# Performance work log

Hardware: AMD Instinct MI355X
Metric: run time of the kernel (lower is better)

The kernel has to match this reference:

```python
import jax, jax.numpy as jnp
import numpy as np

B, N, C_IN, C_EMB, G = 16, 1024, 16, 64, 128
NEG = -1e12


def _lap(m):
    # m @ D^-1/2, transpose, @ D^-1/2  (matches torch code incl. transpose)
    d = jnp.sum(m, axis=1) ** -0.5
    return (m * d[None, :]).T * d[None, :]


def setup_inputs():
    key = jax.random.key(0)
    ks = jax.random.split(key, 16)
    f = jax.random.normal
    return {
        'x': f(ks[0], (B, C_IN, N), jnp.float32),
        'ct': f(ks[1], (B, C_EMB, N), jnp.float32),
        'graph_data': jax.random.uniform(ks[2], (2, N, N), dtype=jnp.float32),
        'emb_w': f(ks[3], (C_EMB, C_IN)) / np.sqrt(C_IN).astype(np.float32),
        'emb_b': f(ks[4], (C_EMB,)) * 0.01,
        'emb2_w': f(ks[5], (N, N)) / np.sqrt(N).astype(np.float32),
        'emb2_b': f(ks[6], (N,)) * 0.01,
        'att_W': f(ks[7], (C_EMB, C_EMB)) / np.sqrt(C_EMB).astype(np.float32),
        'att_a': f(ks[8], (2 * C_EMB, 1)) / np.sqrt(2 * C_EMB).astype(np.float32),
        'att_GL': f(ks[9], (N, G)) / np.sqrt(G).astype(np.float32),
        'uai_w': f(ks[10], (C_EMB, C_EMB)) / np.sqrt(C_EMB).astype(np.float32),
        'uai_b': f(ks[11], (C_EMB,)) * 0.01,
        'lin1_w': f(ks[12], (C_EMB, C_EMB)) / np.sqrt(C_EMB).astype(np.float32),
        'lin2_w': f(ks[13], (C_EMB, C_EMB)) / np.sqrt(C_EMB).astype(np.float32),
        'lin2_b': f(ks[14], (C_EMB,)) * 0.01,
        'ln_w': jnp.ones((C_EMB, N), jnp.float32),
        'ln_b': jnp.zeros((C_EMB, N), jnp.float32),
    }


def reference(x, ct, graph_data, emb_w, emb_b, emb2_w, emb2_b, att_W, att_a,
              att_GL, uai_w, uai_b, lin1_w, lin2_w, lin2_b, ln_w, ln_b):
    # emb: Conv1d k=1 -> leaky_relu -> Linear over node axis N
    h0 = jax.nn.leaky_relu(jnp.einsum('bcn,ec->ben', x, emb_w) + emb_b[None, :, None])
    h0 = jnp.einsum('ben,mn->bem', h0, emb2_w) + emb2_b[None, None, :]
    inp = jnp.swapaxes(h0, 1, 2)  # [B,N,C']

    # InterpositionAttention (repeat/cat factorized: e_ij = leakyrelu(a1.h_i + a2.h_j))
    eye = jnp.eye(N, dtype=x.dtype)
    adj_att = jax.nn.softmax(jax.nn.relu(att_GL @ att_GL.T), axis=-1) + eye
    h = inp @ att_W  # [B,N,C']
    e = jax.nn.leaky_relu((h @ att_a[:C_EMB]) + jnp.swapaxes(h @ att_a[C_EMB:], 1, 2))  # [B,N,N]
    att = jax.nn.softmax(jnp.where(adj_att > 0, e, NEG), axis=2)
    x_att = jnp.swapaxes(jax.nn.relu(att @ h), 1, 2)  # [B,C',N]

    # UAI module (eval mode: dropout off -> all MC samples equal -> sigma = 0)
    mu = jnp.swapaxes(x_att, 1, 2) @ uai_w.T + uai_b  # [B,N,C']
    x_uai = jnp.swapaxes(mu, 1, 2)  # [B,C',N]

    g1 = _lap(graph_data[0] + eye)
    g2 = _lap(graph_data[1] + eye)

    # learned adjacency from pairwise squared distances (cdist p=2, squared)
    xf = jnp.swapaxes(x_uai, 1, 2)  # [B,N,C']
    sq = jnp.sum(xf * xf, axis=-1)
    d2 = jnp.maximum(sq[:, :, None] + sq[:, None, :] - 2.0 * (xf @ jnp.swapaxes(xf, 1, 2)), 0.0)
    gl = jax.nn.softmax(jnp.exp(-d2 / (2.0 * C_EMB)) + eye, axis=-1)  # sigma^2 = emb_size

    def ln(z):  # LayerNorm over last two dims [C', N]
        m = jnp.mean(z, axis=(1, 2), keepdims=True)
        v = jnp.var(z, axis=(1, 2), keepdims=True)
        return (z - m) / jnp.sqrt(v + 1e-5) * ln_w + ln_b

    l1 = lambda z: jnp.einsum('oc,bcn->bon', lin1_w, z)
    l2 = lambda z: jnp.einsum('oc,bcn->bon', lin2_w, z) + lin2_b[None, :, None]

    x_new = ln(l1(x_uai) @ gl + l1(l1(x_uai) @ g1) @ g2)
    ft = jax.nn.gelu(ln(l2(x_uai) @ gl + l2(l2(x_uai) @ g1) @ g2), approximate=False)
    rt = ft  # rt is computed by the identical expression (dropout off)

    ct_new = ft * ct + x_new - ft * x_new
    ht = rt * jax.nn.elu(ct_new) + x_uai - rt * x_uai
    return (ht, ct_new)
```

## Files before the change

### kernel.cpp

```cpp
#include <hip/hip_runtime.h>
#include <math.h>

typedef unsigned short u16;
typedef __attribute__((ext_vector_type(8))) short short8;
typedef __attribute__((ext_vector_type(4))) float floatx4;

constexpr int BATCH = 16;
constexpr int NI = 1024;
constexpr int CE = 64;
constexpr int CI = 16;
constexpr long long NN2  = (long long)NI * NI;
constexpr long long BCN  = (long long)BATCH * CE * NI;
constexpr long long BNv  = (long long)BATCH * NI;
constexpr long long BNN  = (long long)BATCH * NI * NI;
constexpr long long S1 = (long long)CE * NI;
constexpr long long S2 = 2 * S1;

__device__ __forceinline__ float lrelu01(float x) { return x > 0.f ? x : 0.01f * x; }

__device__ __forceinline__ u16 f2bf(float f) {
  unsigned u = __builtin_bit_cast(unsigned, f);
  return (u16)((u + 0x7fffu + ((u >> 16) & 1u)) >> 16);
}
__device__ __forceinline__ float bf2f(u16 h) {
  unsigned u = ((unsigned)h) << 16;
  return __builtin_bit_cast(float, u);
}
__device__ __forceinline__ unsigned fkey(float f) {
  unsigned u = __builtin_bit_cast(unsigned, f);
  return (u & 0x80000000u) ? ~u : (u | 0x80000000u);
}
__device__ __forceinline__ float funkey(unsigned k) {
  unsigned u = (k & 0x80000000u) ? (k & 0x7fffffffu) : ~k;
  return __builtin_bit_cast(float, u);
}

template<int BM, int BN, int MODE>
__global__ __launch_bounds__(256) void mgemm(
    const u16* __restrict__ Ag, const u16* __restrict__ B1g, const u16* __restrict__ B2g,
    int K1, int K, int lda, int ldb, long long bsA, long long bsB1,
    float* __restrict__ Cf, u16* __restrict__ Cb, int ldc, long long bsC,
    const float* __restrict__ aux1, const float* __restrict__ aux2,
    const float* __restrict__ aux3, const float* __restrict__ aux4,
    float* __restrict__ Zout)
{
  constexpr int RM = BM / 2, RN = BN / 2, MI = RM / 16, NJ = RN / 16;
  __shared__ __align__(16) u16 As[BM * 64];
  __shared__ __align__(16) u16 Bs[BN * 64];
  const int z = blockIdx.z;
  const int n0 = blockIdx.x * BN;
  const int r0 = blockIdx.y * BM;
  const u16* Ab = Ag + (long long)z * bsA + (long long)r0 * lda;
  const u16* Bb1 = B1g + (long long)z * bsB1 + (long long)n0 * ldb;
  const int tid = threadIdx.x;
  const int lane = tid & 63;
  const int wid = tid >> 6;
  const int wr = wid >> 1, wc = wid & 1;
  const int q = lane >> 4, mlow = lane & 15;

  floatx4 acc[MI][NJ] = {};

  for (int k0 = 0; k0 < K; k0 += 64) {
    const u16* Asrc = Ab + k0;
    const u16* Bsrc = (k0 < K1) ? (Bb1 + k0)
                                : (B2g + (long long)n0 * ldb + (k0 - K1));
#pragma unroll
    for (int s = 0; s < (BM * 8) / 256; s++) {
      int cid = tid + s * 256;
      int r = cid >> 3, craw = cid & 7;
      uint4 v = *(const uint4*)(Asrc + (long long)r * lda + craw * 8);
      *(uint4*)&As[(r * 8 + (craw ^ (r & 7))) * 8] = v;
    }
#pragma unroll
    for (int s = 0; s < (BN * 8) / 256; s++) {
      int cid = tid + s * 256;
      int r = cid >> 3, craw = cid & 7;
      uint4 v = *(const uint4*)(Bsrc + (long long)r * ldb + craw * 8);
      *(uint4*)&Bs[(r * 8 + (craw ^ (r & 7))) * 8] = v;
    }
    __syncthreads();
#pragma unroll
    for (int kh = 0; kh < 2; kh++) {
      const int kc = kh * 4 + q;
      short8 afr[MI], bfr[NJ];
#pragma unroll
      for (int i = 0; i < MI; i++) {
        int row = wr * RM + i * 16 + mlow;
        afr[i] = *(const short8*)&As[(row * 8 + (kc ^ (row & 7))) * 8];
      }
#pragma unroll
      for (int j = 0; j < NJ; j++) {
        int row = wc * RN + j * 16 + mlow;
        bfr[j] = *(const short8*)&Bs[(row * 8 + (kc ^ (row & 7))) * 8];
      }
#pragma unroll
      for (int i = 0; i < MI; i++)
#pragma unroll
        for (int j = 0; j < NJ; j++)
          acc[i][j] = __builtin_amdgcn_mfma_f32_16x16x32_bf16(afr[i], bfr[j], acc[i][j], 0, 0, 0);
    }
    __syncthreads();
  }

  if constexpr (MODE == 3) {
    const float* sqb = aux1 + (long long)z * NI;
#pragma unroll
    for (int i = 0; i < MI; i++) {
#pragma unroll
      for (int rg = 0; rg < 4; rg++) {
        int r = r0 + wr * RM + i * 16 + q * 4 + rg;
        float sqi = sqb[r];
        float rsum = 0.f;
#pragma unroll
        for (int j = 0; j < NJ; j++) {
          int ncol = n0 + wc * RN + j * 16 + mlow;
          float d2 = fmaxf(sqi + sqb[ncol] - 2.f * acc[i][j][rg], 0.f);
          float w = __expf(__expf(-d2 * (1.f / 128.f)) + (r == ncol ? 1.f : 0.f) - 2.f);
          Cb[(long long)z * bsC + (long long)r * ldc + ncol] = f2bf(w);
          rsum += w;
        }
        rsum += __shfl_xor(rsum, 1);
        rsum += __shfl_xor(rsum, 2);
        rsum += __shfl_xor(rsum, 4);
        rsum += __shfl_xor(rsum, 8);
        if (mlow == 0) atomicAdd(&Zout[(long long)z * NI + r], rsum);
      }
    }
  } else if constexpr (MODE == 2) {
#pragma unroll
    for (int i = 0; i < MI; i++) {
#pragma unroll
      for (int rg = 0; rg < 4; rg++) {
        int r = r0 + wr * RM + i * 16 + q * 4 + rg;
        float sqp = 0.f;
#pragma unroll
        for (int j = 0; j < NJ; j++) {
          int ncol = n0 + wc * RN + j * 16 + mlow;
          float v = acc[i][j][rg] + aux1[ncol];
          long long ix = (long long)z * bsC + (long long)r * ldc + ncol;
          Cf[ix] = v;
          Cb[ix] = f2bf(v);
          sqp = fmaf(v, v, sqp);
        }
        sqp += __shfl_xor(sqp, 1);
        sqp += __shfl_xor(sqp, 2);
        sqp += __shfl_xor(sqp, 4);
        sqp += __shfl_xor(sqp, 8);
        if (mlow == 0) atomicAdd(&Zout[(long long)z * NI + r], sqp);
      }
    }
  } else {
#pragma unroll
    for (int i = 0; i < MI; i++) {
#pragma unroll
      for (int j = 0; j < NJ; j++) {
#pragma unroll
        for (int rg = 0; rg < 4; rg++) {
          int r = r0 + wr * RM + i * 16 + q * 4 + rg;
          int ncol = n0 + wc * RN + j * 16 + mlow;
          float v = acc[i][j][rg];
          if constexpr (MODE == 1) {
            v *= aux1[(long long)z * NI + r];
            v = fmaxf(v, 0.f);
            Cb[(long long)z * bsC + (long long)r * ldc + ncol] = f2bf(v);
          } else if constexpr (MODE == 4) {
            int blk = r >> 6, oo = r & 63;
            int drow = ((blk & 1) << 6) + oo;
            if (blk < 2) v = v / aux1[(long long)z * NI + ncol];
            Cb[(long long)z * bsC + (long long)drow * 2048 + (long long)(blk >> 1) * 1024 + ncol] =
                f2bf(v);
          } else if constexpr (MODE == 5) {
            v += aux3[r] * aux1[(long long)z * NI + ncol] + aux4[r] * aux2[ncol];
            Cf[(long long)z * bsC + (long long)r * ldc + ncol] = v;
          } else if constexpr (MODE == 6) {
            Cb[(long long)z * bsC + (long long)r * ldc + ncol] = f2bf(v);
          } else if constexpr (MODE == 9) {
            v += aux3[r];
            Cb[(long long)z * bsC + (long long)r * ldc + ncol] = f2bf(v);
          }
        }
      }
    }
  }
}

__global__ __launch_bounds__(256) void lap_rowsum(const float* __restrict__ gd,
                                                  float* __restrict__ dr)
{
  const int ki = blockIdx.x;
  const float* row = gd + (long long)ki * NI;
  float s = 0.f;
  for (int j = threadIdx.x; j < NI; j += 256) s += row[j];
  __shared__ float red[256];
  red[threadIdx.x] = s; __syncthreads();
  for (int st = 128; st > 0; st >>= 1) {
    if (threadIdx.x < st) red[threadIdx.x] += red[threadIdx.x + st];
    __syncthreads();
  }
  if (threadIdx.x == 0) dr[ki] = rsqrtf(red[0] + 1.f);
}

__global__ __launch_bounds__(256) void mega_prep(
    const float* __restrict__ l1w, const float* __restrict__ l2w,
    const float* __restrict__ l2b, const float* __restrict__ uaiw,
    const float* __restrict__ attW,
    u16* __restrict__ stack4, float* __restrict__ rb2ext, float* __restrict__ rl2ext,
    u16* __restrict__ uaiw_bf, u16* __restrict__ attwT_bf,
    const float* __restrict__ emb2w, u16* __restrict__ emb2w_bf,
    const float* __restrict__ x, const float* __restrict__ ew,
    const float* __restrict__ eb, u16* __restrict__ h0a,
    const float* __restrict__ gd, const float* __restrict__ dsum,
    u16* __restrict__ g2t, u16* __restrict__ g1,
    float* __restrict__ cs1)
{
  __shared__ float sm[1088];
  const int bid = blockIdx.x;
  const int t = threadIdx.x;
  if (bid < 97) {
    const int gid = bid * 256 + t;
    if (gid < 4096) {
      stack4[gid] = f2bf(l1w[gid]);
    } else if (gid < 8192) {
      stack4[gid] = f2bf(l2w[gid - 4096]);
    } else if (gid < 12288) {
      int tt = gid - 8192, o = tt >> 6, m = tt & 63;
      float s = 0.f;
      for (int c = 0; c < 64; c++) s = fmaf(l1w[o * 64 + c], l1w[c * 64 + m], s);
      stack4[gid] = f2bf(s);
    } else if (gid < 16384) {
      int tt = gid - 12288, o = tt >> 6, m = tt & 63;
      float s = 0.f;
      for (int c = 0; c < 64; c++) s = fmaf(l2w[o * 64 + c], l2w[c * 64 + m], s);
      stack4[gid] = f2bf(s);
    } else if (gid < 16512) {
      int r = gid - 16384;
      rb2ext[r] = (r < 64) ? 0.f : l2b[r - 64];
    } else if (gid < 16640) {
      int r = gid - 16512;
      float v = 0.f;
      if (r >= 64) { int o = r - 64; for (int c = 0; c < 64; c++) v = fmaf(l2w[o * 64 + c], l2b[c], v); }
      rl2ext[r] = v;
    } else if (gid < 20736) {
      uaiw_bf[gid - 16640] = f2bf(uaiw[gid - 16640]);
    } else if (gid < 24832) {
      int idx = gid - 20736;
      int k = idx >> 6, e = idx & 63;
      attwT_bf[idx] = f2bf(attW[e * 64 + k]);
    }
  } else if (bid < 4193) {
    const long long i = (long long)(bid - 97) * 256 + t;
    emb2w_bf[i] = f2bf(emb2w[i]);
  } else if (bid < 5217) {
    const int be = bid - 4193;
    const int b = be >> 6, e = be & 63;
    float* w = sm;
    if (t < CI) w[t] = ew[e * CI + t];
    __syncthreads();
    const float bias = eb[e];
    const float* xb = x + (long long)b * CI * NI;
    u16* outp = h0a + (long long)be * NI;
    for (int n = t; n < NI; n += 256) {
      float a = bias;
#pragma unroll
      for (int c = 0; c < CI; c++) a = fmaf(xb[c * NI + n], w[c], a);
      outp[n] = f2bf(lrelu01(a));
    }
  } else if (bid < 9313) {
    const long long idx = (long long)(bid - 5217) * 256 + t;
    const int m = (int)(idx >> 10), j = (int)(idx & 1023);
    const float* d = dsum + NI;
    float v = (gd[NN2 + idx] + (m == j ? 1.f : 0.f)) * d[m] * d[j];
    g2t[idx] = f2bf(v);
  } else if (bid < 10337) {
    const int sub = bid - 9313;
    const int bx = (sub & 31) * 32, by = (sub >> 5) * 32;
    const int lx = t & 31, ly = t >> 5;
    float* tile = sm;
    for (int yy = ly; yy < 32; yy += 8)
      tile[yy * 33 + lx] = gd[(long long)(by + yy) * NI + bx + lx];
    __syncthreads();
    for (int yy = ly; yy < 32; yy += 8) {
      const int i = bx + yy, j = by + lx;
      float v = (tile[lx * 33 + yy] + (i == j ? 1.f : 0.f)) * dsum[i] * dsum[j];
      g1[(long long)i * NI + j] = f2bf(v);
    }
  } else {
    const int n = bid - 10337;
    float s = 0.f;
    for (int i = t; i < NI; i += 256) s = fmaf(gd[(long long)n * NI + i], dsum[i], s);
    float* red = sm;
    red[t] = s; __syncthreads();
    for (int st = 128; st > 0; st >>= 1) {
      if (t < st) red[t] += red[t + st];
      __syncthreads();
    }
    if (t == 0) cs1[n] = dsum[n] * (red[0] + dsum[n]);
  }
}

__global__ __launch_bounds__(256) void csv2_kernel(const float* __restrict__ gd1,
                                                   const float* __restrict__ d,
                                                   const float* __restrict__ cs1,
                                                   float* __restrict__ cs2,
                                                   float* __restrict__ v2)
{
  const int m = blockIdx.x;
  float s = 0.f, sv = 0.f;
  for (int n = threadIdx.x; n < NI; n += 256) {
    float g = gd1[(long long)m * NI + n] * d[n];
    s += g;
    sv = fmaf(g, cs1[n], sv);
  }
  __shared__ float r1[256], r2[256];
  r1[threadIdx.x] = s; r2[threadIdx.x] = sv; __syncthreads();
  for (int st = 128; st > 0; st >>= 1) {
    if (threadIdx.x < st) { r1[threadIdx.x] += r1[threadIdx.x + st]; r2[threadIdx.x] += r2[threadIdx.x + st]; }
    __syncthreads();
  }
  if (threadIdx.x == 0) {
    cs2[m] = d[m] * (r1[0] + d[m]);
    v2[m] = d[m] * (r2[0] + d[m] * cs1[m]);
  }
}

__global__ __launch_bounds__(256) void s12_kernel(const u16* __restrict__ hTb,
                                                  const float* __restrict__ atta,
                                                  float* __restrict__ s1,
                                                  float* __restrict__ s2,
                                                  unsigned* __restrict__ s2mU)
{
  const int b = blockIdx.y;
  const int n = blockIdx.x * 256 + threadIdx.x;
  const u16* base = hTb + (long long)b * S1 + n;
  float v1 = 0.f, v2 = 0.f;
#pragma unroll 8
  for (int c = 0; c < 64; c++) {
    float h = bf2f(base[(long long)c * NI]);
    v1 = fmaf(h, atta[c], v1);
    v2 = fmaf(h, atta[64 + c], v2);
  }
  s1[(long long)b * NI + n] = v1;
  s2[(long long)b * NI + n] = v2;
  float mx = v2;
  for (int off = 1; off < 64; off <<= 1) mx = fmaxf(mx, __shfl_xor(mx, off));
  if ((threadIdx.x & 63) == 0) atomicMax(&s2mU[b], fkey(mx));
}

__global__ __launch_bounds__(256) void att_p(const float* __restrict__ s1,
                                             const float* __restrict__ s2,
                                             const unsigned* __restrict__ s2mU,
                                             u16* __restrict__ Wp,
                                             float* __restrict__ invZatt)
{
  const int b = blockIdx.y;
  const int wid = threadIdx.x >> 6, lane = threadIdx.x & 63;
  const int i = blockIdx.x * 4 + wid;
  const float s1i = s1[(long long)b * NI + i];
  const float m = lrelu01(s1i + funkey(s2mU[b]));
  const float* s2b = s2 + (long long)b * NI;
  u16* row = Wp + (long long)b * NN2 + (long long)i * NI;
  float lsum = 0.f;
#pragma unroll
  for (int it = 0; it < 4; it++) {
    const int j0 = it * 256 + lane * 4;
    float4 sv = *(const float4*)(s2b + j0);
    float p0 = __expf(lrelu01(s1i + sv.x) - m);
    float p1 = __expf(lrelu01(s1i + sv.y) - m);
    float p2 = __expf(lrelu01(s1i + sv.z) - m);
    float p3 = __expf(lrelu01(s1i + sv.w) - m);
    uint2 pk;
    pk.x = (unsigned)f2bf(p0) | ((unsigned)f2bf(p1) << 16);
    pk.y = (unsigned)f2bf(p2) | ((unsigned)f2bf(p3) << 16);
    *(uint2*)(row + j0) = pk;
    lsum += p0 + p1 + p2 + p3;
  }
  for (int off = 1; off < 64; off <<= 1) lsum += __shfl_xor(lsum, off);
  if (lane == 0) invZatt[(long long)b * NI + i] = 1.f / lsum;
}

__global__ __launch_bounds__(256) void cc_kernel(const u16* __restrict__ W,
                                                 const float* __restrict__ Zgl,
                                                 const float* __restrict__ cs2,
                                                 float* __restrict__ cc)
{
  const int b = blockIdx.y;
  const int wid = threadIdx.x >> 6, lane = threadIdx.x & 63;
  const int m = blockIdx.x * 4 + wid;
  const u16* row = W + (long long)b * NN2 + (long long)m * NI;
  const float* zz = Zgl + (long long)b * NI;
  float s = 0.f;
#pragma unroll
  for (int it = 0; it < 4; it++) {
    const int j0 = it * 256 + lane * 4;
    uint2 pk = *(const uint2*)(row + j0);
    float4 zv = *(const float4*)(zz + j0);
    s += bf2f((u16)(pk.x & 0xffff)) / zv.x + bf2f((u16)(pk.x >> 16)) / zv.y
       + bf2f((u16)(pk.y & 0xffff)) / zv.z + bf2f((u16)(pk.y >> 16)) / zv.w;
  }
  for (int off = 1; off < 64; off <<= 1) s += __shfl_xor(s, off);
  if (lane == 0) cc[(long long)b * NI + m] = s + cs2[m];
}

__global__ __launch_bounds__(256) void ln_reduce(const float* __restrict__ T,
                                                 float* __restrict__ stats)
{
  const int b = blockIdx.x, half = blockIdx.y, chunk = blockIdx.z;
  const float* z = T + (long long)b * S2 + (long long)half * S1 + (long long)chunk * 4096;
  float s = 0.f, ss = 0.f;
#pragma unroll
  for (int it = 0; it < 4; it++) {
    float4 v = *(const float4*)(z + it * 1024 + threadIdx.x * 4);
    s += v.x + v.y + v.z + v.w;
    ss = fmaf(v.x, v.x, ss); ss = fmaf(v.y, v.y, ss);
    ss = fmaf(v.z, v.z, ss); ss = fmaf(v.w, v.w, ss);
  }
  for (int off = 1; off < 64; off <<= 1) {
    s += __shfl_xor(s, off);
    ss += __shfl_xor(ss, off);
  }
  __shared__ float r1[4], r2[4];
  const int wid = threadIdx.x >> 6, lane = threadIdx.x & 63;
  if (lane == 0) { r1[wid] = s; r2[wid] = ss; }
  __syncthreads();
  if (threadIdx.x == 0) {
    atomicAdd(&stats[b * 2 + half], r1[0] + r1[1] + r1[2] + r1[3]);
    atomicAdd(&stats[32 + b * 2 + half], r2[0] + r2[1] + r2[2] + r2[3]);
  }
}

__global__ __launch_bounds__(256) void ln_final_t(const float* __restrict__ T,
                                                  const float* __restrict__ stats,
                                                  const float* __restrict__ lnw,
                                                  const float* __restrict__ lnb,
                                                  const float* __restrict__ ct,
                                                  const float* __restrict__ xuT,
                                                  float* __restrict__ outp)
{
  __shared__ float xs[64 * 65];
  const int blk = blockIdx.x;
  const int b = blk >> 4;
  const int n0 = (blk & 15) << 6;
  const int t = threadIdx.x;
  const int tc = t & 63, tr = t >> 6;
#pragma unroll
  for (int i = 0; i < 16; i++) {
    int nn = i * 4 + tr;
    xs[tc * 65 + nn] = xuT[((long long)b << 16) + (long long)(n0 + nn) * 64 + tc];
  }
  __syncthreads();
  const float inv_n = 1.f / 65536.f;
  const float m0 = stats[b * 2] * inv_n;
  const float m1 = stats[b * 2 + 1] * inv_n;
  const float rs0 = rsqrtf(fmaxf(stats[32 + b * 2] * inv_n - m0 * m0, 0.f) + 1e-5f);
  const float rs1 = rsqrtf(fmaxf(stats[32 + b * 2 + 1] * inv_n - m1 * m1, 0.f) + 1e-5f);
#pragma unroll
  for (int j = 0; j < 16; j++) {
    const int c = j * 4 + tr;
    const int n = n0 + tc;
    const int rem = c * NI + n;
    const long long toff = (long long)b * S2 + rem;
    const float t0 = T[toff];
    const float t1 = T[toff + S1];
    const float w = lnw[rem], bb = lnb[rem];
    const float xn = (t0 - m0) * rs0 * w + bb;
    float ft = (t1 - m1) * rs1 * w + bb;
    ft = 0.5f * ft * (1.f + erff(ft * 0.70710678118654752f));
    const float u = xs[c * 65 + tc];
    const long long oidx = ((long long)b << 16) + rem;
    const float cn = fmaf(ft, ct[oidx] - xn, xn);
    const float el = cn > 0.f ? cn : expm1f(cn);
    outp[oidx] = fmaf(ft, el - u, u);
    outp[BCN + oidx] = cn;
  }
}

extern "C" void kernel_launch(void* const* d_in, const int* in_sizes, int n_in,
                              void* d_out, int out_size, void* d_ws, size_t ws_size,
                              hipStream_t stream)
{
  (void)in_sizes; (void)n_in; (void)out_size; (void)ws_size;
  const float* x      = (const float*)d_in[0];
  const float* ct     = (const float*)d_in[1];
  const float* gdata  = (const float*)d_in[2];
  const float* emb_w  = (const float*)d_in[3];
  const float* emb_b  = (const float*)d_in[4];
  const float* emb2_w = (const float*)d_in[5];
  const float* emb2_b = (const float*)d_in[6];
  const float* att_W  = (const float*)d_in[7];
  const float* att_a  = (const float*)d_in[8];
  const float* uai_w  = (const float*)d_in[10];
  const float* uai_b  = (const float*)d_in[11];
  const float* lin1_w = (const float*)d_in[12];
  const float* lin2_w = (const float*)d_in[13];
  const float* lin2_b = (const float*)d_in[14];
  const float* ln_w   = (const float*)d_in[15];
  const float* ln_b   = (const float*)d_in[16];
  float* outp = (float*)d_out;

  float* ws = (float*)d_ws;
  long long o = 0;
  auto af = [&](long long n) { float* p = ws + o; o += (n + 63) & ~63LL; return p; };
  auto au = [&](long long n) { return (u16*)af((n + 1) / 2); };

  float* Tacc    = af(S2 * BATCH);
  float* xuaiTf  = af(S1 * BATCH);
  float* s1      = af(BNv);
  float* s2      = af(BNv);
  float* invZatt = af(BNv);
  float* dsum    = af(2 * NI);
  float* cs1v    = af(NI);
  float* cs2v    = af(NI);
  float* v2v     = af(NI);
  float* ccv     = af(BNv);
  float* rb2ext  = af(128);
  float* rl2ext  = af(128);
  float* zeroreg = af(2 * BNv + 80);
  float* Zgl     = zeroreg;
  float* sqv     = zeroreg + BNv;
  float* stats   = zeroreg + 2 * BNv;
  unsigned* s2mU = (unsigned*)(stats + 64);
  u16* emb2w_bf  = au(NN2);
  u16* h0a_bf    = au(S1 * BATCH);
  u16* h0Tb      = au(S1 * BATCH);
  u16* hTb       = au(S1 * BATCH);
  u16* xattb     = au(S1 * BATCH);
  u16* xuaiTb    = au(S1 * BATCH);
  u16* g1b       = au(NN2);
  u16* g2tb      = au(NN2);
  u16* G12b      = au(NN2);
  u16* Abig      = au((long long)BATCH * 128 * 2048);
  u16* stack4    = au(256 * 64);
  u16* uaiw_bf   = au(CE * CE);
  u16* attwT_bf  = au(CE * CE);
  u16* bigW      = au(BNN);

  hipMemsetAsync(zeroreg, 0, (2 * BNv + 80) * sizeof(float), stream);

  lap_rowsum<<<2 * NI, 256, 0, stream>>>(gdata, dsum);

  mega_prep<<<11361, 256, 0, stream>>>(
      lin1_w, lin2_w, lin2_b, uai_w, att_W,
      stack4, rb2ext, rl2ext, uaiw_bf, attwT_bf,
      emb2_w, emb2w_bf, x, emb_w, emb_b, h0a_bf,
      gdata, dsum, g2tb, g1b, cs1v);

  csv2_kernel<<<NI, 256, 0, stream>>>(gdata + NN2, dsum + NI, cs1v, cs2v, v2v);

  mgemm<64, 64, 6><<<dim3(16, 16, 1), 256, 0, stream>>>(
      g2tb, g1b, nullptr, NI, NI, NI, NI, 0, 0,
      nullptr, G12b, NI, 0, nullptr, nullptr, nullptr, nullptr, nullptr);

  mgemm<64, 64, 9><<<dim3(1, 16, BATCH), 256, 0, stream>>>(
      emb2w_bf, h0a_bf, nullptr, NI, NI, NI, NI, 0, S1,
      nullptr, h0Tb, CE, S1, nullptr, nullptr, emb2_b, nullptr, nullptr);

  mgemm<64, 64, 6><<<dim3(16, 1, BATCH), 256, 0, stream>>>(
      attwT_bf, h0Tb, nullptr, CE, CE, CE, CE, 0, S1,
      nullptr, hTb, NI, S1, nullptr, nullptr, nullptr, nullptr, nullptr);

  s12_kernel<<<dim3(4, BATCH), 256, 0, stream>>>(hTb, att_a, s1, s2, s2mU);
  att_p<<<dim3(NI / 4, BATCH), 256, 0, stream>>>(s1, s2, s2mU, bigW, invZatt);

  mgemm<64, 64, 1><<<dim3(1, 16, BATCH), 256, 0, stream>>>(
      bigW, hTb, nullptr, NI, NI, NI, NI, NN2, S1,
      nullptr, xattb, CE, S1, invZatt, nullptr, nullptr, nullptr, nullptr);

  mgemm<64, 64, 2><<<dim3(1, 16, BATCH), 256, 0, stream>>>(
      xattb, uaiw_bf, nullptr, CE, CE, CE, CE, S1, 0,
      xuaiTf, xuaiTb, CE, S1, uai_b, nullptr, nullptr, nullptr, sqv);

  mgemm<128, 128, 3><<<dim3(8, 8, BATCH), 256, 0, stream>>>(
      xuaiTb, xuaiTb, nullptr, CE, CE, CE, CE, S1, S1,
      nullptr, bigW, NI, NN2, sqv, nullptr, nullptr, nullptr, Zgl);

  cc_kernel<<<dim3(NI / 4, BATCH), 256, 0, stream>>>(bigW, Zgl, cs2v, ccv);

  mgemm<64, 64, 4><<<dim3(16, 4, BATCH), 256, 0, stream>>>(
      stack4, xuaiTb, nullptr, CE, CE, CE, CE, 0, S1,
      nullptr, Abig, 0, (long long)128 * 2048, Zgl, nullptr, nullptr, nullptr, nullptr);

  mgemm<64, 128, 5><<<dim3(8, 2, BATCH), 256, 0, stream>>>(
      Abig, bigW, G12b, NI, 2 * NI, 2048, NI, (long long)128 * 2048, NN2,
      Tacc, nullptr, NI, S2, ccv, v2v, rb2ext, rl2ext, nullptr);

  ln_reduce<<<dim3(BATCH, 2, 16), 256, 0, stream>>>(Tacc, stats);
  ln_final_t<<<256, 256, 0, stream>>>(Tacc, stats, ln_w, ln_b, ct, xuaiTf, outp);
}
```

Measured before the change: 274.5 us.

## Fuse attention probability generation into GEMM and fold score/LN stats into epilogues

The attention GEMM now builds the exp-softmax numerators on the fly in its A-tile load instead of reading a materialized B×N×N bf16 matrix. The att_a projections are precomputed as W·a vectors, so s1/s2 and the s2 max come out of the emb2 GEMM epilogue, and the s12 kernel is removed. LayerNorm sum and sum-of-squares are accumulated in the final GEMM epilogue, dropping the ln_reduce pass. The fp32 x_uai copy is also dropped in favour of the bf16 copy. This removes a large global write/read of the attention matrix at the cost of recomputing exp per tile, plus extra bf16 rounding in the residual path.

```diff
diff --git a/kernel.cpp b/kernel.cpp
--- a/kernel.cpp
+++ b/kernel.cpp
@@ -61,22 +61,54 @@
   floatx4 acc[MI][NJ] = {};
 
   for (int k0 = 0; k0 < K; k0 += 64) {
-    const u16* Asrc = Ab + k0;
-    const u16* Bsrc = (k0 < K1) ? (Bb1 + k0)
-                                : (B2g + (long long)n0 * ldb + (k0 - K1));
-#pragma unroll
-    for (int s = 0; s < (BM * 8) / 256; s++) {
-      int cid = tid + s * 256;
-      int r = cid >> 3, craw = cid & 7;
-      uint4 v = *(const uint4*)(Asrc + (long long)r * lda + craw * 8);
-      *(uint4*)&As[(r * 8 + (craw ^ (r & 7))) * 8] = v;
-    }
-#pragma unroll
-    for (int s = 0; s < (BN * 8) / 256; s++) {
-      int cid = tid + s * 256;
-      int r = cid >> 3, craw = cid & 7;
-      uint4 v = *(const uint4*)(Bsrc + (long long)r * ldb + craw * 8);
-      *(uint4*)&Bs[(r * 8 + (craw ^ (r & 7))) * 8] = v;
+    if constexpr (MODE == 10) {
+      const float* s1z = aux2 + (long long)z * NI;
+      const float* s2z = aux3 + (long long)z * NI;
+      const float mb = funkey(((const unsigned*)Zout)[z]);
+#pragma unroll
+      for (int s = 0; s < (BM * 8) / 256; s++) {
+        int cid = tid + s * 256;
+        int r = cid >> 3, craw = cid & 7;
+        float s1r = s1z[r0 + r];
+        float mr = lrelu01(s1r + mb);
+        const float* sp = s2z + k0 + craw * 8;
+        float4 sa = *(const float4*)sp;
+        float4 sb = *(const float4*)(sp + 4);
+        float p0 = __expf(lrelu01(s1r + sa.x) - mr);
+        float p1 = __expf(lrelu01(s1r + sa.y) - mr);
+        float p2 = __expf(lrelu01(s1r + sa.z) - mr);
+        float p3 = __expf(lrelu01(s1r + sa.w) - mr);
+        float p4 = __expf(lrelu01(s1r + sb.x) - mr);
+        float p5 = __expf(lrelu01(s1r + sb.y) - mr);
+        float p6 = __expf(lrelu01(s1r + sb.z) - mr);
+        float p7 = __expf(lrelu01(s1r + sb.w) - mr);
+        uint4 v;
+        v.x = (unsigned)f2bf(p0) | ((unsigned)f2bf(p1) << 16);
+        v.y = (unsigned)f2bf(p2) | ((unsigned)f2bf(p3) << 16);
+        v.z = (unsigned)f2bf(p4) | ((unsigned)f2bf(p5) << 16);
+        v.w = (unsigned)f2bf(p6) | ((unsigned)f2bf(p7) << 16);
+        *(uint4*)&As[(r * 8 + (craw ^ (r & 7))) * 8] = v;
+      }
+    } else {
+      const u16* Asrc = Ab + k0;
+#pragma unroll
+      for (int s = 0; s < (BM * 8) / 256; s++) {
+        int cid = tid + s * 256;
+        int r = cid >> 3, craw = cid & 7;
+        uint4 v = *(const uint4*)(Asrc + (long long)r * lda + craw * 8);
+        *(uint4*)&As[(r * 8 + (craw ^ (r & 7))) * 8] = v;
+      }
+    }
+    {
+      const u16* Bsrc = (k0 < K1) ? (Bb1 + k0)
+                                  : (B2g + (long long)n0 * ldb + (k0 - K1));
+#pragma unroll
+      for (int s = 0; s < (BN * 8) / 256; s++) {
+        int cid = tid + s * 256;
+        int r = cid >> 3, craw = cid & 7;
+        uint4 v = *(const uint4*)(Bsrc + (long long)r * ldb + craw * 8);
+        *(uint4*)&Bs[(r * 8 + (craw ^ (r & 7))) * 8] = v;
+      }
     }
     __syncthreads();
 #pragma unroll
@@ -137,9 +169,7 @@
         for (int j = 0; j < NJ; j++) {
           int ncol = n0 + wc * RN + j * 16 + mlow;
           float v = acc[i][j][rg] + aux1[ncol];
-          long long ix = (long long)z * bsC + (long long)r * ldc + ncol;
-          Cf[ix] = v;
-          Cb[ix] = f2bf(v);
+          Cb[(long long)z * bsC + (long long)r * ldc + ncol] = f2bf(v);
           sqp = fmaf(v, v, sqp);
         }
         sqp += __shfl_xor(sqp, 1);
@@ -149,7 +179,43 @@
         if (mlow == 0) atomicAdd(&Zout[(long long)z * NI + r], sqp);
       }
     }
+  } else if constexpr (MODE == 11) {
+    float* sred = (float*)As;
+#pragma unroll
+    for (int i = 0; i < MI; i++) {
+#pragma unroll
+      for (int rg = 0; rg < 4; rg++) {
+        int rloc = wr * RM + i * 16 + q * 4 + rg;
+        int r = r0 + rloc;
+        float rb = aux3[r];
+        float ps1 = 0.f, ps2 = 0.f;
+#pragma unroll
+        for (int j = 0; j < NJ; j++) {
+          int ncol = n0 + wc * RN + j * 16 + mlow;
+          float v = acc[i][j][rg] + rb;
+          Cb[(long long)z * bsC + (long long)r * ldc + ncol] = f2bf(v);
+          ps1 = fmaf(v, aux1[ncol], ps1);
+          ps2 = fmaf(v, aux2[ncol], ps2);
+        }
+        ps1 += __shfl_xor(ps1, 1); ps1 += __shfl_xor(ps1, 2);
+        ps1 += __shfl_xor(ps1, 4); ps1 += __shfl_xor(ps1, 8);
+        ps2 += __shfl_xor(ps2, 1); ps2 += __shfl_xor(ps2, 2);
+        ps2 += __shfl_xor(ps2, 4); ps2 += __shfl_xor(ps2, 8);
+        if (mlow == 0) { sred[rloc * 2 + wc] = ps1; sred[128 + rloc * 2 + wc] = ps2; }
+      }
+    }
+    __syncthreads();
+    if (tid < 64) {
+      float v1 = sred[tid * 2] + sred[tid * 2 + 1];
+      float v2 = sred[128 + tid * 2] + sred[128 + tid * 2 + 1];
+      Cf[(long long)z * NI + r0 + tid] = v1;
+      Zout[(long long)z * NI + r0 + tid] = v2;
+      float mx = v2;
+      for (int off = 1; off < 64; off <<= 1) mx = fmaxf(mx, __shfl_xor(mx, off));
+      if (tid == 0) atomicMax((unsigned*)B2g + z, fkey(mx));
+    }
   } else {
+    float ts = 0.f, tss = 0.f;
 #pragma unroll
     for (int i = 0; i < MI; i++) {
 #pragma unroll
@@ -159,7 +225,7 @@
           int r = r0 + wr * RM + i * 16 + q * 4 + rg;
           int ncol = n0 + wc * RN + j * 16 + mlow;
           float v = acc[i][j][rg];
-          if constexpr (MODE == 1) {
+          if constexpr (MODE == 10) {
             v *= aux1[(long long)z * NI + r];
             v = fmaxf(v, 0.f);
             Cb[(long long)z * bsC + (long long)r * ldc + ncol] = f2bf(v);
@@ -172,13 +238,26 @@
           } else if constexpr (MODE == 5) {
             v += aux3[r] * aux1[(long long)z * NI + ncol] + aux4[r] * aux2[ncol];
             Cf[(long long)z * bsC + (long long)r * ldc + ncol] = v;
+            ts += v;
+            tss = fmaf(v, v, tss);
           } else if constexpr (MODE == 6) {
-            Cb[(long long)z * bsC + (long long)r * ldc + ncol] = f2bf(v);
-          } else if constexpr (MODE == 9) {
-            v += aux3[r];
             Cb[(long long)z * bsC + (long long)r * ldc + ncol] = f2bf(v);
           }
         }
+      }
+    }
+    if constexpr (MODE == 5) {
+      float* red = (float*)As;
+      red[tid] = ts; red[256 + tid] = tss;
+      __syncthreads();
+      for (int st = 128; st > 0; st >>= 1) {
+        if (tid < st) { red[tid] += red[tid + st]; red[256 + tid] += red[256 + tid + st]; }
+        __syncthreads();
+      }
+      if (tid == 0) {
+        const int half = r0 >> 6;
+        atomicAdd(&Zout[z * 2 + half], red[0]);
+        atomicAdd(&Zout[32 + z * 2 + half], red[256]);
       }
     }
   }
@@ -203,9 +282,9 @@
 __global__ __launch_bounds__(256) void mega_prep(
     const float* __restrict__ l1w, const float* __restrict__ l2w,
     const float* __restrict__ l2b, const float* __restrict__ uaiw,
-    const float* __restrict__ attW,
+    const float* __restrict__ attW, const float* __restrict__ atta,
     u16* __restrict__ stack4, float* __restrict__ rb2ext, float* __restrict__ rl2ext,
-    u16* __restrict__ uaiw_bf, u16* __restrict__ attwT_bf,
+    u16* __restrict__ uaiw_bf, u16* __restrict__ attwT_bf, float* __restrict__ w12,
     const float* __restrict__ emb2w, u16* __restrict__ emb2w_bf,
     const float* __restrict__ x, const float* __restrict__ ew,
     const float* __restrict__ eb, u16* __restrict__ h0a,
@@ -216,7 +295,7 @@
   __shared__ float sm[1088];
   const int bid = blockIdx.x;
   const int t = threadIdx.x;
-  if (bid < 97) {
+  if (bid < 98) {
     const int gid = bid * 256 + t;
     if (gid < 4096) {
       stack4[gid] = f2bf(l1w[gid]);
@@ -246,12 +325,18 @@
       int idx = gid - 20736;
       int k = idx >> 6, e = idx & 63;
       attwT_bf[idx] = f2bf(attW[e * 64 + k]);
-    }
-  } else if (bid < 4193) {
-    const long long i = (long long)(bid - 97) * 256 + t;
+    } else if (gid < 24960) {
+      int c = gid - 24832;
+      int cc = c & 63, which = c >> 6;
+      float s = 0.f;
+      for (int k = 0; k < 64; k++) s = fmaf(attW[cc * 64 + k], atta[which * 64 + k], s);
+      w12[c] = s;
+    }
+  } else if (bid < 4194) {
+    const long long i = (long long)(bid - 98) * 256 + t;
     emb2w_bf[i] = f2bf(emb2w[i]);
-  } else if (bid < 5217) {
-    const int be = bid - 4193;
+  } else if (bid < 5218) {
+    const int be = bid - 4194;
     const int b = be >> 6, e = be & 63;
     float* w = sm;
     if (t < CI) w[t] = ew[e * CI + t];
@@ -265,14 +350,14 @@
       for (int c = 0; c < CI; c++) a = fmaf(xb[c * NI + n], w[c], a);
       outp[n] = f2bf(lrelu01(a));
     }
-  } else if (bid < 9313) {
-    const long long idx = (long long)(bid - 5217) * 256 + t;
+  } else if (bid < 9314) {
+    const long long idx = (long long)(bid - 5218) * 256 + t;
     const int m = (int)(idx >> 10), j = (int)(idx & 1023);
     const float* d = dsum + NI;
     float v = (gd[NN2 + idx] + (m == j ? 1.f : 0.f)) * d[m] * d[j];
     g2t[idx] = f2bf(v);
-  } else if (bid < 10337) {
-    const int sub = bid - 9313;
+  } else if (bid < 10338) {
+    const int sub = bid - 9314;
     const int bx = (sub & 31) * 32, by = (sub >> 5) * 32;
     const int lx = t & 31, ly = t >> 5;
     float* tile = sm;
@@ -285,7 +370,7 @@
       g1[(long long)i * NI + j] = f2bf(v);
     }
   } else {
-    const int n = bid - 10337;
+    const int n = bid - 10338;
     float s = 0.f;
     for (int i = t; i < NI; i += 256) s = fmaf(gd[(long long)n * NI + i], dsum[i], s);
     float* red = sm;
@@ -323,33 +408,9 @@
   }
 }
 
-__global__ __launch_bounds__(256) void s12_kernel(const u16* __restrict__ hTb,
-                                                  const float* __restrict__ atta,
-                                                  float* __restrict__ s1,
-                                                  float* __restrict__ s2,
-                                                  unsigned* __restrict__ s2mU)
-{
-  const int b = blockIdx.y;
-  const int n = blockIdx.x * 256 + threadIdx.x;
-  const u16* base = hTb + (long long)b * S1 + n;
-  float v1 = 0.f, v2 = 0.f;
-#pragma unroll 8
-  for (int c = 0; c < 64; c++) {
-    float h = bf2f(base[(long long)c * NI]);
-    v1 = fmaf(h, atta[c], v1);
-    v2 = fmaf(h, atta[64 + c], v2);
-  }
-  s1[(long long)b * NI + n] = v1;
-  s2[(long long)b * NI + n] = v2;
-  float mx = v2;
-  for (int off = 1; off < 64; off <<= 1) mx = fmaxf(mx, __shfl_xor(mx, off));
-  if ((threadIdx.x & 63) == 0) atomicMax(&s2mU[b], fkey(mx));
-}
-
-__global__ __launch_bounds__(256) void att_p(const float* __restrict__ s1,
+__global__ __launch_bounds__(256) void att_z(const float* __restrict__ s1,
                                              const float* __restrict__ s2,
                                              const unsigned* __restrict__ s2mU,
-                                             u16* __restrict__ Wp,
                                              float* __restrict__ invZatt)
 {
   const int b = blockIdx.y;
@@ -358,21 +419,13 @@
   const float s1i = s1[(long long)b * NI + i];
   const float m = lrelu01(s1i + funkey(s2mU[b]));
   const float* s2b = s2 + (long long)b * NI;
-  u16* row = Wp + (long long)b * NN2 + (long long)i * NI;
   float lsum = 0.f;
 #pragma unroll
   for (int it = 0; it < 4; it++) {
     const int j0 = it * 256 + lane * 4;
     float4 sv = *(const float4*)(s2b + j0);
-    float p0 = __expf(lrelu01(s1i + sv.x) - m);
-    float p1 = __expf(lrelu01(s1i + sv.y) - m);
-    float p2 = __expf(lrelu01(s1i + sv.z) - m);
-    float p3 = __expf(lrelu01(s1i + sv.w) - m);
-    uint2 pk;
-    pk.x = (unsigned)f2bf(p0) | ((unsigned)f2bf(p1) << 16);
-    pk.y = (unsigned)f2bf(p2) | ((unsigned)f2bf(p3) << 16);
-    *(uint2*)(row + j0) = pk;
-    lsum += p0 + p1 + p2 + p3;
+    lsum += __expf(lrelu01(s1i + sv.x) - m) + __expf(lrelu01(s1i + sv.y) - m)
+          + __expf(lrelu01(s1i + sv.z) - m) + __expf(lrelu01(s1i + sv.w) - m);
   }
   for (int off = 1; off < 64; off <<= 1) lsum += __shfl_xor(lsum, off);
   if (lane == 0) invZatt[(long long)b * NI + i] = 1.f / lsum;
@@ -401,39 +454,12 @@
   if (lane == 0) cc[(long long)b * NI + m] = s + cs2[m];
 }
 
-__global__ __launch_bounds__(256) void ln_reduce(const float* __restrict__ T,
-                                                 float* __restrict__ stats)
-{
-  const int b = blockIdx.x, half = blockIdx.y, chunk = blockIdx.z;
-  const float* z = T + (long long)b * S2 + (long long)half * S1 + (long long)chunk * 4096;
-  float s = 0.f, ss = 0.f;
-#pragma unroll
-  for (int it = 0; it < 4; it++) {
-    float4 v = *(const float4*)(z + it * 1024 + threadIdx.x * 4);
-    s += v.x + v.y + v.z + v.w;
-    ss = fmaf(v.x, v.x, ss); ss = fmaf(v.y, v.y, ss);
-    ss = fmaf(v.z, v.z, ss); ss = fmaf(v.w, v.w, ss);
-  }
-  for (int off = 1; off < 64; off <<= 1) {
-    s += __shfl_xor(s, off);
-    ss += __shfl_xor(ss, off);
-  }
-  __shared__ float r1[4], r2[4];
-  const int wid = threadIdx.x >> 6, lane = threadIdx.x & 63;
-  if (lane == 0) { r1[wid] = s; r2[wid] = ss; }
-  __syncthreads();
-  if (threadIdx.x == 0) {
-    atomicAdd(&stats[b * 2 + half], r1[0] + r1[1] + r1[2] + r1[3]);
-    atomicAdd(&stats[32 + b * 2 + half], r2[0] + r2[1] + r2[2] + r2[3]);
-  }
-}
-
 __global__ __launch_bounds__(256) void ln_final_t(const float* __restrict__ T,
                                                   const float* __restrict__ stats,
                                                   const float* __restrict__ lnw,
                                                   const float* __restrict__ lnb,
                                                   const float* __restrict__ ct,
-                                                  const float* __restrict__ xuT,
+                                                  const u16* __restrict__ xuT,
                                                   float* __restrict__ outp)
 {
   __shared__ float xs[64 * 65];
@@ -445,7 +471,7 @@
 #pragma unroll
   for (int i = 0; i < 16; i++) {
     int nn = i * 4 + tr;
-    xs[tc * 65 + nn] = xuT[((long long)b << 16) + (long long)(n0 + nn) * 64 + tc];
+    xs[tc * 65 + nn] = bf2f(xuT[((long long)b << 16) + (long long)(n0 + nn) * 64 + tc]);
   }
   __syncthreads();
   const float inv_n = 1.f / 65536.f;
@@ -503,7 +529,6 @@
   auto au = [&](long long n) { return (u16*)af((n + 1) / 2); };
 
   float* Tacc    = af(S2 * BATCH);
-  float* xuaiTf  = af(S1 * BATCH);
   float* s1      = af(BNv);
   float* s2      = af(BNv);
   float* invZatt = af(BNv);
@@ -514,6 +539,7 @@
   float* ccv     = af(BNv);
   float* rb2ext  = af(128);
   float* rl2ext  = af(128);
+  float* w12     = af(128);
   float* zeroreg = af(2 * BNv + 80);
   float* Zgl     = zeroreg;
   float* sqv     = zeroreg + BNv;
@@ -538,9 +564,9 @@
 
   lap_rowsum<<<2 * NI, 256, 0, stream>>>(gdata, dsum);
 
-  mega_prep<<<11361, 256, 0, stream>>>(
-      lin1_w, lin2_w, lin2_b, uai_w, att_W,
-      stack4, rb2ext, rl2ext, uaiw_bf, attwT_bf,
+  mega_prep<<<11362, 256, 0, stream>>>(
+      lin1_w, lin2_w, lin2_b, uai_w, att_W, att_a,
+      stack4, rb2ext, rl2ext, uaiw_bf, attwT_bf, w12,
       emb2_w, emb2w_bf, x, emb_w, emb_b, h0a_bf,
       gdata, dsum, g2tb, g1b, cs1v);
 
@@ -550,24 +576,23 @@
       g2tb, g1b, nullptr, NI, NI, NI, NI, 0, 0,
       nullptr, G12b, NI, 0, nullptr, nullptr, nullptr, nullptr, nullptr);
 
-  mgemm<64, 64, 9><<<dim3(1, 16, BATCH), 256, 0, stream>>>(
-      emb2w_bf, h0a_bf, nullptr, NI, NI, NI, NI, 0, S1,
-      nullptr, h0Tb, CE, S1, nullptr, nullptr, emb2_b, nullptr, nullptr);
+  mgemm<64, 64, 11><<<dim3(1, 16, BATCH), 256, 0, stream>>>(
+      emb2w_bf, h0a_bf, (const u16*)s2mU, NI, NI, NI, NI, 0, S1,
+      s1, h0Tb, CE, S1, w12, w12 + 64, emb2_b, nullptr, s2);
+
+  att_z<<<dim3(NI / 4, BATCH), 256, 0, stream>>>(s1, s2, s2mU, invZatt);
 
   mgemm<64, 64, 6><<<dim3(16, 1, BATCH), 256, 0, stream>>>(
       attwT_bf, h0Tb, nullptr, CE, CE, CE, CE, 0, S1,
       nullptr, hTb, NI, S1, nullptr, nullptr, nullptr, nullptr, nullptr);
 
-  s12_kernel<<<dim3(4, BATCH), 256, 0, stream>>>(hTb, att_a, s1, s2, s2mU);
-  att_p<<<dim3(NI / 4, BATCH), 256, 0, stream>>>(s1, s2, s2mU, bigW, invZatt);
-
-  mgemm<64, 64, 1><<<dim3(1, 16, BATCH), 256, 0, stream>>>(
-      bigW, hTb, nullptr, NI, NI, NI, NI, NN2, S1,
-      nullptr, xattb, CE, S1, invZatt, nullptr, nullptr, nullptr, nullptr);
+  mgemm<64, 64, 10><<<dim3(1, 16, BATCH), 256, 0, stream>>>(
+      hTb, hTb, nullptr, NI, NI, NI, NI, 0, S1,
+      nullptr, xattb, CE, S1, invZatt, s1, s2, nullptr, (float*)s2mU);
 
   mgemm<64, 64, 2><<<dim3(1, 16, BATCH), 256, 0, stream>>>(
       xattb, uaiw_bf, nullptr, CE, CE, CE, CE, S1, 0,
-      xuaiTf, xuaiTb, CE, S1, uai_b, nullptr, nullptr, nullptr, sqv);
+      nullptr, xuaiTb, CE, S1, uai_b, nullptr, nullptr, nullptr, sqv);
 
   mgemm<128, 128, 3><<<dim3(8, 8, BATCH), 256, 0, stream>>>(
       xuaiTb, xuaiTb, nullptr, CE, CE, CE, CE, S1, S1,
@@ -581,8 +606,7 @@
 
   mgemm<64, 128, 5><<<dim3(8, 2, BATCH), 256, 0, stream>>>(
       Abig, bigW, G12b, NI, 2 * NI, 2048, NI, (long long)128 * 2048, NN2,
-      Tacc, nullptr, NI, S2, ccv, v2v, rb2ext, rl2ext, nullptr);
-
-  ln_reduce<<<dim3(BATCH, 2, 16), 256, 0, stream>>>(Tacc, stats);
-  ln_final_t<<<256, 256, 0, stream>>>(Tacc, stats, ln_w, ln_b, ct, xuaiTf, outp);
-}
+      Tacc, nullptr, NI, S2, ccv, v2v, rb2ext, rl2ext, stats);
+
+  ln_final_t<<<256, 256, 0, stream>>>(Tacc, stats, ln_w, ln_b, ct, xuaiTb, outp);
+}
```

Result: no change. 269.8 us (-1.7%).
